# Kernel tuning notes

Hardware: AMD Instinct MI355X
Metric: run time of the kernel (lower is better)

Reference implementation:

```python
import jax, jax.numpy as jnp
import numpy as np

DIM = 128
CODEBOOK_SIZE = 1024


def setup_inputs() -> dict:
    key = jax.random.key(0)
    kx, ke = jax.random.split(key)
    x = jax.random.normal(kx, (16, 4096, DIM), dtype=jnp.float32)
    # kaiming_uniform_ on (codebook_size, dim): bound = sqrt(6 / fan_in), fan_in = dim
    bound = float(np.sqrt(6.0 / DIM))
    embed = jax.random.uniform(ke, (CODEBOOK_SIZE, DIM), dtype=jnp.float32,
                               minval=-bound, maxval=bound)
    return {"x": x, "embed": embed}


def reference(x, embed):
    orig_shape = x.shape
    flat = x.reshape(-1, x.shape[-1])                     # [N, D]
    x2 = jnp.sum(flat * flat, axis=1, keepdims=True)      # [N, 1]
    e2 = jnp.sum(embed * embed, axis=1)                   # [K]
    dist = -(x2 - 2.0 * (flat @ embed.T) + e2[None, :])   # [N, K]
    embed_ind = jnp.argmax(dist, axis=-1)                 # [N]
    embed_ind = embed_ind.reshape(orig_shape[:-1])        # [B, S]
    quantize = jnp.take(embed, embed_ind, axis=0)         # [B, S, D]
    return quantize, embed_ind
```

## Files before the change

kernel.cpp:

```cpp
#include <hip/hip_runtime.h>

#define DIM     128
#define NCODES  1024
#define TILE_M  64
#define LDSS    136
#define DELTA   0.02f
#define RPB     4
#define RGRID   1024

typedef __attribute__((ext_vector_type(8))) _Float16 half8;
typedef __attribute__((ext_vector_type(4))) _Float16 half4;
typedef __attribute__((ext_vector_type(4))) float    f32x4;


__global__ __launch_bounds__(256) void prep_kernel(
    const float* __restrict__ embed, double* __restrict__ e2d,
    float* __restrict__ e2f, _Float16* __restrict__ eh, int* __restrict__ cnt)
{
  if (blockIdx.x == 0 && threadIdx.x == 0) *cnt = 0;
  const int w = threadIdx.x >> 6;
  const int l = threadIdx.x & 63;
  const int c = blockIdx.x * 4 + w;
  const float* row = embed + (size_t)c * DIM;
  float v0 = row[l], v1 = row[l + 64];
  eh[(size_t)c * DIM + l]      = (_Float16)v0;
  eh[(size_t)c * DIM + 64 + l] = (_Float16)v1;
  double sq = (double)v0 * v0 + (double)v1 * v1;
  #pragma unroll
  for (int off = 32; off >= 1; off >>= 1) sq += __shfl_down(sq, off, 64);
  if (l == 0) { e2d[c] = sq; e2f[c] = (float)sq; }
}

__global__ __launch_bounds__(256) void transpose_kernel(
    const float* __restrict__ embed, float* __restrict__ embedT)
{
  __shared__ float tile[64][65];
  const int c0 = blockIdx.y * 64;
  const int k0 = blockIdx.x * 64;
  const int t = threadIdx.x;
  #pragma unroll
  for (int i = 0; i < 16; ++i) {
    int idx = t + i * 256;
    int r = idx >> 6, c = idx & 63;
    tile[r][c] = embed[(size_t)(c0 + r) * DIM + k0 + c];
  }
  __syncthreads();
  #pragma unroll
  for (int i = 0; i < 16; ++i) {
    int idx = t + i * 256;
    int r = idx >> 6, c = idx & 63;
    embedT[(size_t)(k0 + r) * NCODES + c0 + c] = tile[c][r];
  }
}

__global__ __launch_bounds__(256)
__attribute__((amdgpu_waves_per_eu(4, 4)))
void pass1_kernel(
    const float* __restrict__ x, const float* __restrict__ embed,
    const _Float16* __restrict__ eh, const float* __restrict__ e2f,
    float* __restrict__ outQ, float* __restrict__ outIdx,
    int* __restrict__ cnt, int* __restrict__ list)
{
  __shared__ _Float16 xh[TILE_M * LDSS];
  __shared__ float rb_best[4][TILE_M];
  __shared__ float rb_sec [4][TILE_M];
  __shared__ int   fidx[TILE_M];

  const int tid  = threadIdx.x;
  const int row0 = blockIdx.x * TILE_M;

  {
    const f32x4* x4 = (const f32x4*)(x + (size_t)row0 * DIM);
    #pragma unroll
    for (int i = 0; i < 8; ++i) {
      int e = tid + i * 256;
      int r = e >> 5, c4 = e & 31;
      f32x4 v = x4[e];
      half4 h;
      h[0] = (_Float16)v[0]; h[1] = (_Float16)v[1];
      h[2] = (_Float16)v[2]; h[3] = (_Float16)v[3];
      *(half4*)&xh[r * LDSS + c4 * 4] = h;
    }
  }
  __syncthreads();

  const int l  = tid & 63, w = tid >> 6;
  const int rl = l & 15,  q = l >> 4;
  const int col0 = q * 8;
  const int abase0 = rl * LDSS + col0;

  float bestp[16], secp[16];
  #pragma unroll
  for (int s = 0; s < 16; ++s) { bestp[s] = 3.0e38f; secp[s] = 3.3e38f; }

  const int codeBase = w * 256;
  const _Float16* ehw = eh + (size_t)(codeBase + rl) * DIM + col0;

  half8 bbuf[2][4];
  float e2buf[2];
  #pragma unroll
  for (int ks = 0; ks < 4; ++ks) bbuf[0][ks] = *(const half8*)(ehw + ks * 32);
  e2buf[0] = e2f[codeBase + rl];

  #pragma unroll 2
  for (int ch = 0; ch < 16; ++ch) {
    const int cur = ch & 1, nxt = cur ^ 1;
    const int mycode = codeBase + ch * 16 + rl;
    if (ch < 15) {
      const _Float16* ehn = ehw + (size_t)(ch + 1) * (16 * DIM);
      #pragma unroll
      for (int ks = 0; ks < 4; ++ks) bbuf[nxt][ks] = *(const half8*)(ehn + ks * 32);
      e2buf[nxt] = e2f[mycode + 16];
    }
    const float e2c = e2buf[cur];

    int ozero = 0;
    asm volatile("" : "+v"(ozero));
    const int ab = abase0 + ozero;

    #pragma unroll
    for (int m = 0; m < 4; ++m) {
      f32x4 acc = (f32x4){0.f, 0.f, 0.f, 0.f};
      #pragma unroll
      for (int ks = 0; ks < 4; ++ks) {
        half8 af = *(const half8*)&xh[ab + m * (16 * LDSS) + ks * 32];
        acc = __builtin_amdgcn_mfma_f32_16x16x32_f16(af, bbuf[cur][ks], acc, 0, 0, 0);
      }
      #pragma unroll
      for (int r = 0; r < 4; ++r) {
        const int s = m * 4 + r;
        float sc  = fmaf(-2.0f, acc[r], e2c);
        float scp = __int_as_float((__float_as_int(sc) & ~1023) | mycode);
        secp[s]  = fminf(secp[s], fmaxf(bestp[s], scp));
        bestp[s] = fminf(bestp[s], scp);
      }
    }
  }

  #pragma unroll
  for (int off = 1; off < 16; off <<= 1) {
    #pragma unroll
    for (int s = 0; s < 16; ++s) {
      float ob = __shfl_xor(bestp[s], off, 16);
      float os = __shfl_xor(secp[s],  off, 16);
      float mx = fmaxf(bestp[s], ob);
      bestp[s] = fminf(bestp[s], ob);
      secp[s]  = fminf(fminf(secp[s], os), mx);
    }
  }
  if (rl == 0) {
    #pragma unroll
    for (int m = 0; m < 4; ++m)
      #pragma unroll
      for (int r = 0; r < 4; ++r) {
        int s = m * 4 + r;
        int row = m * 16 + q * 4 + r;
        rb_best[w][row] = bestp[s];
        rb_sec [w][row] = secp[s];
      }
  }
  __syncthreads();

  if (tid < TILE_M) {
    float bv = rb_best[0][tid], sv = rb_sec[0][tid];
    #pragma unroll
    for (int ww = 1; ww < 4; ++ww) {
      float ob = rb_best[ww][tid], os = rb_sec[ww][tid];
      float mx = fmaxf(bv, ob);
      bv = fminf(bv, ob);
      sv = fminf(fminf(sv, os), mx);
    }
    int bi = __float_as_int(bv) & 1023;
    int grow = row0 + tid;
    outIdx[grow] = (float)bi;
    fidx[tid] = bi;
    if (sv - bv <= DELTA + fabsf(bv) * 4.8828125e-4f) {
      int p = atomicAdd(cnt, 1);
      list[p] = grow;
    }
  }
  __syncthreads();

  {
    const f32x4* E4   = (const f32x4*)embed;
    f32x4*       out4 = (f32x4*)(outQ + (size_t)row0 * DIM);
    #pragma unroll
    for (int i = 0; i < 8; ++i) {
      int e = tid + i * 256;
      int r = e >> 5, c4 = e & 31;
      out4[e] = E4[fidx[r] * 32 + c4];
    }
  }
}

__global__ __launch_bounds__(256) void refine2_kernel(
    const float* __restrict__ x, const float* __restrict__ embed,
    const float* __restrict__ embedT,
    const double* __restrict__ e2d, const float* __restrict__ e2f,
    float* __restrict__ outQ, float* __restrict__ outIdx,
    const int* __restrict__ cnt, const int* __restrict__ list)
{
  __shared__ f32x4 xst[DIM];
  __shared__ float rb1[RPB][4], rb2[RPB][4];
  __shared__ int   ri1[RPB][4], ri2[RPB][4];
  __shared__ int   cand[RPB][2];

  const int t = threadIdx.x;
  const int l = t & 63, w = t >> 6;
  const int n = *cnt;
  float* xsf = (float*)xst;

  for (int base = blockIdx.x * RPB; base < n; base += RGRID * RPB) {
    const int nr = min(RPB, n - base);
    #pragma unroll
    for (int i = 0; i < 2; ++i) {
      int idx = t + i * 256;
      int r = idx >> 7, k = idx & 127;
      float v = 0.f;
      if (r < nr) v = x[(size_t)list[base + r] * DIM + k];
      xsf[k * RPB + r] = v;
    }
    __syncthreads();

    f32x4 dot[RPB];
    #pragma unroll
    for (int r = 0; r < RPB; ++r) dot[r] = (f32x4){0.f, 0.f, 0.f, 0.f};
    const f32x4* eT4 = (const f32x4*)embedT;
    #pragma unroll 4
    for (int k = 0; k < DIM; ++k) {
      f32x4 e4  = eT4[k * 256 + t];
      f32x4 xk4 = xst[k];
      #pragma unroll
      for (int r = 0; r < RPB; ++r) {
        dot[r][0] = fmaf(xk4[r], e4[0], dot[r][0]);
        dot[r][1] = fmaf(xk4[r], e4[1], dot[r][1]);
        dot[r][2] = fmaf(xk4[r], e4[2], dot[r][2]);
        dot[r][3] = fmaf(xk4[r], e4[3], dot[r][3]);
      }
    }

    #pragma unroll
    for (int r = 0; r < RPB; ++r) {
      float b1 = 3.4e38f, b2 = 3.4e38f; int i1 = 0, i2 = 0;
      #pragma unroll
      for (int j = 0; j < 4; ++j) {
        int c = 4 * t + j;
        float sc = fmaf(-2.0f, dot[r][j], e2f[c]);
        bool better = (sc < b1);
        float lv = better ? b1 : sc;  int li = better ? i1 : c;
        if (better) { b1 = sc; i1 = c; }
        bool t2 = (lv < b2) || (lv == b2 && li < i2);
        if (t2) { b2 = lv; i2 = li; }
      }
      #pragma unroll
      for (int off = 1; off < 64; off <<= 1) {
        float o1 = __shfl_xor(b1, off, 64); int oi1 = __shfl_xor(i1, off, 64);
        float o2 = __shfl_xor(b2, off, 64); int oi2 = __shfl_xor(i2, off, 64);
        bool take = (o1 < b1) || (o1 == b1 && oi1 < i1);
        float n1 = take ? o1 : b1; int ni1 = take ? oi1 : i1;
        float lo = take ? b1 : o1; int loi = take ? i1 : oi1;
        float c2v = take ? o2 : b2; int c2i = take ? oi2 : i2;
        bool u2 = (c2v < lo) || (c2v == lo && c2i < loi);
        b1 = n1; i1 = ni1;
        b2 = u2 ? c2v : lo; i2 = u2 ? c2i : loi;
      }
      if (l == 0) { rb1[r][w] = b1; ri1[r][w] = i1; rb2[r][w] = b2; ri2[r][w] = i2; }
    }
    __syncthreads();

    if (t < RPB) {
      float v1 = rb1[t][0], v2 = rb2[t][0]; int j1 = ri1[t][0], j2 = ri2[t][0];
      #pragma unroll
      for (int ww = 1; ww < 4; ++ww) {
        float o1 = rb1[t][ww], o2 = rb2[t][ww]; int oi1 = ri1[t][ww], oi2 = ri2[t][ww];
        bool take = (o1 < v1) || (o1 == v1 && oi1 < j1);
        float n1 = take ? o1 : v1; int ni1 = take ? oi1 : j1;
        float lo = take ? v1 : o1; int loi = take ? j1 : oi1;
        float c2v = take ? o2 : v2; int c2i = take ? oi2 : j2;
        bool u2 = (c2v < lo) || (c2v == lo && c2i < loi);
        v1 = n1; j1 = ni1; v2 = u2 ? c2v : lo; j2 = u2 ? c2i : loi;
      }
      cand[t][0] = j1; cand[t][1] = j2;
    }
    __syncthreads();

    if (w < nr) {
      int c1 = cand[w][0], c2 = cand[w][1];
      float xa = xsf[l * RPB + w], xb = xsf[(l + 64) * RPB + w];
      double p1 = (double)xa * (double)embed[(size_t)c1 * DIM + l]
                + (double)xb * (double)embed[(size_t)c1 * DIM + 64 + l];
      double p2 = (double)xa * (double)embed[(size_t)c2 * DIM + l]
                + (double)xb * (double)embed[(size_t)c2 * DIM + 64 + l];
      #pragma unroll
      for (int off = 1; off < 64; off <<= 1) {
        p1 += __shfl_xor(p1, off, 64);
        p2 += __shfl_xor(p2, off, 64);
      }
      double s1 = e2d[c1] - 2.0 * p1;
      double s2 = e2d[c2] - 2.0 * p2;
      int widx = ((s2 < s1) || (s2 == s1 && c2 < c1)) ? c2 : c1;
      int row = list[base + w];
      if (l == 0) outIdx[row] = (float)widx;
      outQ[(size_t)row * DIM + l]      = embed[(size_t)widx * DIM + l];
      outQ[(size_t)row * DIM + 64 + l] = embed[(size_t)widx * DIM + 64 + l];
    }
    __syncthreads();
  }
}

extern "C" void kernel_launch(void* const* d_in, const int* in_sizes, int n_in,
                              void* d_out, int out_size, void* d_ws, size_t ws_size,
                              hipStream_t stream) {
  const float* x     = (const float*)d_in[0];
  const float* embed = (const float*)d_in[1];
  const int N = in_sizes[0] / DIM;

  float* out    = (float*)d_out;
  float* outQ   = out;
  float* outIdx = out + (size_t)N * DIM;

  char* ws = (char*)d_ws;
  double*   e2d  = (double*)  (ws);
  float*    e2f  = (float*)   (ws + 8192);
  _Float16* eh   = (_Float16*)(ws + 12288);
  float*    eT   = (float*)   (ws + 274432);
  int*      cnt  = (int*)     (ws + 798720);
  int*      list = (int*)     (ws + 798976);

  prep_kernel     <<<NCODES / 4, 256, 0, stream>>>(embed, e2d, e2f, eh, cnt);
  dim3 tg(DIM / 64, NCODES / 64);
  transpose_kernel<<<tg,         256, 0, stream>>>(embed, eT);
  pass1_kernel    <<<N / TILE_M, 256, 0, stream>>>(x, embed, eh, e2f, outQ, outIdx, cnt, list);
  refine2_kernel  <<<RGRID,      256, 0, stream>>>(x, embed, eT, e2d, e2f, outQ, outIdx, cnt, list);
}
```

Baseline: 141.5 us.

## Fuse prep and transpose kernels, hoist A fragments to registers, use fmed3

Merges the codebook prep and transpose kernels into one setup kernel, which removes a launch and a second read of the codebook. In pass1 the x-tile MFMA A fragments are loaded once into registers instead of being re-read from LDS for every code chunk. The occupancy hint is relaxed from exactly 4 waves per EU to at least 3, making room for the extra 64 VGPRs of fragments. The best/second-best tracking now uses fmed3 to save ALU ops. Higher register use may lower occupancy, and the setup kernel now runs on only 16 blocks.

```diff
diff --git a/kernel.cpp b/kernel.cpp
--- a/kernel.cpp
+++ b/kernel.cpp
@@ -13,48 +13,58 @@
 typedef __attribute__((ext_vector_type(4))) float    f32x4;
 
 
-__global__ __launch_bounds__(256) void prep_kernel(
+__global__ __launch_bounds__(256) void setup_kernel(
     const float* __restrict__ embed, double* __restrict__ e2d,
-    float* __restrict__ e2f, _Float16* __restrict__ eh, int* __restrict__ cnt)
+    float* __restrict__ e2f, _Float16* __restrict__ eh,
+    float* __restrict__ embedT, int* __restrict__ cnt)
 {
+  __shared__ float tile[64][132];
+  __shared__ double psum[4][64];
   if (blockIdx.x == 0 && threadIdx.x == 0) *cnt = 0;
-  const int w = threadIdx.x >> 6;
-  const int l = threadIdx.x & 63;
-  const int c = blockIdx.x * 4 + w;
-  const float* row = embed + (size_t)c * DIM;
-  float v0 = row[l], v1 = row[l + 64];
-  eh[(size_t)c * DIM + l]      = (_Float16)v0;
-  eh[(size_t)c * DIM + 64 + l] = (_Float16)v1;
-  double sq = (double)v0 * v0 + (double)v1 * v1;
-  #pragma unroll
-  for (int off = 32; off >= 1; off >>= 1) sq += __shfl_down(sq, off, 64);
-  if (l == 0) { e2d[c] = sq; e2f[c] = (float)sq; }
+  const int c0 = blockIdx.x * 64;
+  const int t  = threadIdx.x;
+
+  const f32x4* E4 = (const f32x4*)(embed + (size_t)c0 * DIM);
+  #pragma unroll
+  for (int i = 0; i < 8; ++i) {
+    int e = t + i * 256;
+    int r = e >> 5, c4 = e & 31;
+    f32x4 v = E4[e];
+    *(f32x4*)&tile[r][c4 * 4] = v;
+    half4 h;
+    h[0] = (_Float16)v[0]; h[1] = (_Float16)v[1];
+    h[2] = (_Float16)v[2]; h[3] = (_Float16)v[3];
+    *(half4*)&eh[(size_t)(c0 + r) * DIM + c4 * 4] = h;
+  }
+  __syncthreads();
+
+  {
+    int r = t & 63, part = t >> 6;
+    double s = 0.0;
+    #pragma unroll
+    for (int k = 0; k < 32; ++k) {
+      float v = tile[r][part * 32 + k];
+      s += (double)v * v;
+    }
+    psum[part][r] = s;
+  }
+  __syncthreads();
+  if (t < 64) {
+    double s = psum[0][t] + psum[1][t] + psum[2][t] + psum[3][t];
+    e2d[c0 + t] = s;
+    e2f[c0 + t] = (float)s;
+  }
+
+  #pragma unroll
+  for (int i = 0; i < 32; ++i) {
+    int idx = t + i * 256;
+    int k = idx >> 6, c = idx & 63;
+    embedT[(size_t)k * NCODES + c0 + c] = tile[c][k];
+  }
 }
 
-__global__ __launch_bounds__(256) void transpose_kernel(
-    const float* __restrict__ embed, float* __restrict__ embedT)
-{
-  __shared__ float tile[64][65];
-  const int c0 = blockIdx.y * 64;
-  const int k0 = blockIdx.x * 64;
-  const int t = threadIdx.x;
-  #pragma unroll
-  for (int i = 0; i < 16; ++i) {
-    int idx = t + i * 256;
-    int r = idx >> 6, c = idx & 63;
-    tile[r][c] = embed[(size_t)(c0 + r) * DIM + k0 + c];
-  }
-  __syncthreads();
-  #pragma unroll
-  for (int i = 0; i < 16; ++i) {
-    int idx = t + i * 256;
-    int r = idx >> 6, c = idx & 63;
-    embedT[(size_t)(k0 + r) * NCODES + c0 + c] = tile[c][r];
-  }
-}
-
 __global__ __launch_bounds__(256)
-__attribute__((amdgpu_waves_per_eu(4, 4)))
+__attribute__((amdgpu_waves_per_eu(3)))
 void pass1_kernel(
     const float* __restrict__ x, const float* __restrict__ embed,
     const _Float16* __restrict__ eh, const float* __restrict__ e2f,
@@ -87,7 +97,13 @@
   const int l  = tid & 63, w = tid >> 6;
   const int rl = l & 15,  q = l >> 4;
   const int col0 = q * 8;
-  const int abase0 = rl * LDSS + col0;
+
+  half8 afrag[4][4];
+  #pragma unroll
+  for (int m = 0; m < 4; ++m)
+    #pragma unroll
+    for (int ks = 0; ks < 4; ++ks)
+      afrag[m][ks] = *(const half8*)&xh[(m * 16 + rl) * LDSS + ks * 32 + col0];
 
   float bestp[16], secp[16];
   #pragma unroll
@@ -114,24 +130,18 @@
     }
     const float e2c = e2buf[cur];
 
-    int ozero = 0;
-    asm volatile("" : "+v"(ozero));
-    const int ab = abase0 + ozero;
-
     #pragma unroll
     for (int m = 0; m < 4; ++m) {
       f32x4 acc = (f32x4){0.f, 0.f, 0.f, 0.f};
       #pragma unroll
-      for (int ks = 0; ks < 4; ++ks) {
-        half8 af = *(const half8*)&xh[ab + m * (16 * LDSS) + ks * 32];
-        acc = __builtin_amdgcn_mfma_f32_16x16x32_f16(af, bbuf[cur][ks], acc, 0, 0, 0);
-      }
+      for (int ks = 0; ks < 4; ++ks)
+        acc = __builtin_amdgcn_mfma_f32_16x16x32_f16(afrag[m][ks], bbuf[cur][ks], acc, 0, 0, 0);
       #pragma unroll
       for (int r = 0; r < 4; ++r) {
         const int s = m * 4 + r;
         float sc  = fmaf(-2.0f, acc[r], e2c);
         float scp = __int_as_float((__float_as_int(sc) & ~1023) | mycode);
-        secp[s]  = fminf(secp[s], fmaxf(bestp[s], scp));
+        secp[s]  = __builtin_amdgcn_fmed3f(bestp[s], scp, secp[s]);
         bestp[s] = fminf(bestp[s], scp);
       }
     }
@@ -143,9 +153,8 @@
     for (int s = 0; s < 16; ++s) {
       float ob = __shfl_xor(bestp[s], off, 16);
       float os = __shfl_xor(secp[s],  off, 16);
-      float mx = fmaxf(bestp[s], ob);
+      secp[s]  = fminf(__builtin_amdgcn_fmed3f(bestp[s], ob, secp[s]), os);
       bestp[s] = fminf(bestp[s], ob);
-      secp[s]  = fminf(fminf(secp[s], os), mx);
     }
   }
   if (rl == 0) {
@@ -166,9 +175,8 @@
     #pragma unroll
     for (int ww = 1; ww < 4; ++ww) {
       float ob = rb_best[ww][tid], os = rb_sec[ww][tid];
-      float mx = fmaxf(bv, ob);
+      sv = fminf(__builtin_amdgcn_fmed3f(bv, ob, sv), os);
       bv = fminf(bv, ob);
-      sv = fminf(fminf(sv, os), mx);
     }
     int bi = __float_as_int(bv) & 1023;
     int grow = row0 + tid;
@@ -327,9 +335,7 @@
   int*      cnt  = (int*)     (ws + 798720);
   int*      list = (int*)     (ws + 798976);
 
-  prep_kernel     <<<NCODES / 4, 256, 0, stream>>>(embed, e2d, e2f, eh, cnt);
-  dim3 tg(DIM / 64, NCODES / 64);
-  transpose_kernel<<<tg,         256, 0, stream>>>(embed, eT);
-  pass1_kernel    <<<N / TILE_M, 256, 0, stream>>>(x, embed, eh, e2f, outQ, outIdx, cnt, list);
-  refine2_kernel  <<<RGRID,      256, 0, stream>>>(x, embed, eT, e2d, e2f, outQ, outIdx, cnt, list);
+  setup_kernel  <<<NCODES / 64, 256, 0, stream>>>(embed, e2d, e2f, eh, eT, cnt);
+  pass1_kernel  <<<N / TILE_M,  256, 0, stream>>>(x, embed, eh, e2f, outQ, outIdx, cnt, list);
+  refine2_kernel<<<RGRID,       256, 0, stream>>>(x, embed, eT, e2d, e2f, outQ, outIdx, cnt, list);
 }
```

After: 145.5 us. +2.8%, slower.
